# Kernel optimization log

Hardware: AMD Instinct MI355X
Metric: run time of the kernel (lower is better)

## Reference

```python
import jax, jax.numpy as jnp
import numpy as np

NEG_SLOPE = 0.2  # PyG GATConv default negative_slope


def gat_conv(x, edge_index, W, att_src, att_dst, bias):
    # PyG GATConv, heads=1, add_self_loops=True, lin bias=False, final bias added
    N = x.shape[0]
    h = x @ W                                     # [N, F]
    loops = jnp.arange(N, dtype=edge_index.dtype)
    src = jnp.concatenate([edge_index[0], loops])
    dst = jnp.concatenate([edge_index[1], loops])
    a_src = h @ att_src                           # [N]
    a_dst = h @ att_dst                           # [N]
    e = a_src[src] + a_dst[dst]
    e = jnp.where(e > 0, e, NEG_SLOPE * e)        # leaky_relu
    m = jax.ops.segment_max(e, dst, num_segments=N)
    w = jnp.exp(e - m[dst])
    denom = jax.ops.segment_sum(w, dst, num_segments=N)
    alpha = w / denom[dst]
    out = jax.ops.segment_sum(h[src] * alpha[:, None], dst, num_segments=N)
    return out + bias


def gcn_conv(x, edge_index, W, b):
    # PyG GCNConv: add self-loops + symmetric normalization
    N = x.shape[0]
    loops = jnp.arange(N, dtype=edge_index.dtype)
    src = jnp.concatenate([edge_index[0], loops])
    dst = jnp.concatenate([edge_index[1], loops])
    deg = jax.ops.segment_sum(jnp.ones(src.shape[0], dtype=x.dtype), dst, num_segments=N)
    dinv = jax.lax.rsqrt(jnp.maximum(deg, 1e-12))  # deg >= 1 thanks to self-loops
    norm = dinv[src] * dinv[dst]
    xw = x @ W
    return jax.ops.segment_sum(xw[src] * norm[:, None], dst, num_segments=N) + b


def get_final_node(x, batch, num_graphs):
    nn_ = jax.ops.segment_sum(jnp.ones(x.shape[0], dtype=jnp.int32), batch, num_segments=num_graphs)
    cum = jnp.concatenate([jnp.zeros(1, dtype=nn_.dtype), jnp.cumsum(nn_)[:-1]])
    return x[cum]


def ontology_emb(table, e1, e2, W, asrc, adst, b, idx_map):
    emb = gat_conv(table, e1, W, asrc, adst, b)
    emb = gat_conv(emb, e2, W, asrc, adst, b)
    return emb[idx_map]


def _forward(spec_emb, diag_table, proce_table, atc_table,
             diag_W, diag_asrc, diag_adst, diag_b,
             proce_W, proce_asrc, proce_adst, proce_b,
             atc_W, atc_asrc, atc_adst, atc_b,
             gcn_W1, gcn_b1, gcn_W2, gcn_b2, gcn_W3, gcn_b3,
             diag_e1, diag_e2, proce_e1, proce_e2, atc_e1, atc_e2,
             diag_map, proce_map, atc_map,
             left_x, left_graph_index, right_x, right_graph_index,
             left_x_batch, right_x_batch, num_graphs):
    diag_emb = ontology_emb(diag_table, diag_e1, diag_e2, diag_W, diag_asrc, diag_adst, diag_b, diag_map)
    proce_emb = ontology_emb(proce_table, proce_e1, proce_e2, proce_W, proce_asrc, proce_adst, proce_b, proce_map)
    atc_emb = ontology_emb(atc_table, atc_e1, atc_e2, atc_W, atc_asrc, atc_adst, atc_b, atc_map)
    all_emb = jnp.concatenate([spec_emb, diag_emb, proce_emb, atc_emb], axis=0)
    lh = all_emb[left_x[:, 0]]   # squeeze(dim=1)
    rh = all_emb[right_x[:, 0]]
    for W, b in ((gcn_W1, gcn_b1), (gcn_W2, gcn_b2), (gcn_W3, gcn_b3)):
        lh = gcn_conv(lh, left_graph_index, W, b)
        rh = gcn_conv(rh, right_graph_index, W, b)
    lf = get_final_node(lh, left_x_batch, num_graphs)
    rf = get_final_node(rh, right_x_batch, num_graphs)
    eps = 1e-6  # CosineSimilarity eps
    num = jnp.sum(lf * rf, axis=-1)
    den = jnp.maximum(jnp.linalg.norm(lf, axis=-1), eps) * jnp.maximum(jnp.linalg.norm(rf, axis=-1), eps)
    return num / den


def setup_inputs() -> dict:
    key = jax.random.key(0)
    ks = jax.random.split(key, 32)
    HID = 128
    B, NPG = 2048, 50
    N = B * NPG               # 102400 nodes per side
    E_PAT = 409600            # 4 edges per node
    DIAG_N, DIAG_L = 30000, 20000
    PROCE_N, PROCE_L = 12000, 8000
    ATC_N, ATC_L = 6000, 4000
    ALL = 1 + DIAG_L + PROCE_L + ATC_L
    f = lambda k, s: jax.random.normal(k, s, dtype=jnp.float32)
    scale = 0.1
    inp = {
        'spec_emb': f(ks[0], (1, HID)),
        'diag_table': f(ks[1], (DIAG_N, HID)),
        'proce_table': f(ks[2], (PROCE_N, HID)),
        'atc_table': f(ks[3], (ATC_N, HID)),
    }
    for i, nm in enumerate(['diag', 'proce', 'atc']):
        inp[nm + '_W'] = f(ks[4 + i], (HID, HID)) * scale
        inp[nm + '_asrc'] = f(ks[7 + i], (HID,)) * scale
        inp[nm + '_adst'] = f(ks[10 + i], (HID,)) * scale
        inp[nm + '_b'] = jnp.zeros((HID,), jnp.float32)
    for j in range(3):
        inp['gcn_W%d' % (j + 1)] = f(ks[13 + j], (HID, HID)) * scale
        inp['gcn_b%d' % (j + 1)] = jnp.zeros((HID,), jnp.float32)
    inp['diag_e1'] = jax.random.randint(ks[16], (2, DIAG_N), 0, DIAG_N, dtype=jnp.int32)
    inp['diag_e2'] = jax.random.randint(ks[17], (2, DIAG_N), 0, DIAG_N, dtype=jnp.int32)
    inp['proce_e1'] = jax.random.randint(ks[18], (2, PROCE_N), 0, PROCE_N, dtype=jnp.int32)
    inp['proce_e2'] = jax.random.randint(ks[19], (2, PROCE_N), 0, PROCE_N, dtype=jnp.int32)
    inp['atc_e1'] = jax.random.randint(ks[20], (2, ATC_N), 0, ATC_N, dtype=jnp.int32)
    inp['atc_e2'] = jax.random.randint(ks[21], (2, ATC_N), 0, ATC_N, dtype=jnp.int32)
    inp['diag_map'] = jnp.arange(DIAG_L, dtype=jnp.int32)
    inp['proce_map'] = jnp.arange(PROCE_L, dtype=jnp.int32)
    inp['atc_map'] = jnp.arange(ATC_L, dtype=jnp.int32)
    inp['left_x'] = jax.random.randint(ks[22], (N, 1), 0, ALL, dtype=jnp.int32)
    inp['right_x'] = jax.random.randint(ks[23], (N, 1), 0, ALL, dtype=jnp.int32)
    inp['left_graph_index'] = jax.random.randint(ks[24], (2, E_PAT), 0, N, dtype=jnp.int32)
    inp['right_graph_index'] = jax.random.randint(ks[25], (2, E_PAT), 0, N, dtype=jnp.int32)
    batch = jnp.repeat(jnp.arange(B, dtype=jnp.int32), NPG)
    inp['left_x_batch'] = batch
    inp['right_x_batch'] = batch
    inp['num_graphs'] = B
    return inp


def reference(spec_emb, diag_table, proce_table, atc_table,
              diag_W, diag_asrc, diag_adst, diag_b,
              proce_W, proce_asrc, proce_adst, proce_b,
              atc_W, atc_asrc, atc_adst, atc_b,
              gcn_W1, gcn_b1, gcn_W2, gcn_b2, gcn_W3, gcn_b3,
              diag_e1, diag_e2, proce_e1, proce_e2, atc_e1, atc_e2,
              diag_map, proce_map, atc_map,
              left_x, left_graph_index, right_x, right_graph_index,
              left_x_batch, right_x_batch, num_graphs):
    return _forward(spec_emb, diag_table, proce_table, atc_table,
                    diag_W, diag_asrc, diag_adst, diag_b,
                    proce_W, proce_asrc, proce_adst, proce_b,
                    atc_W, atc_asrc, atc_adst, atc_b,
                    gcn_W1, gcn_b1, gcn_W2, gcn_b2, gcn_W3, gcn_b3,
                    diag_e1, diag_e2, proce_e1, proce_e2, atc_e1, atc_e2,
                    diag_map, proce_map, atc_map,
                    left_x, left_graph_index, right_x, right_graph_index,
                    left_x_batch, right_x_batch, num_graphs)
```

## Files before the change

kernel.cpp:

```cpp
#include <hip/hip_runtime.h>
#include <hip/hip_bf16.h>

#define HID 128

typedef unsigned int uint;
typedef unsigned short ushort;
typedef short short8 __attribute__((ext_vector_type(8)));
typedef float f32x4 __attribute__((ext_vector_type(4)));

static inline int cdiv_i(long a, long b) { return (int)((a + b - 1) / b); }
static inline int imax_i(int a, int b) { return a > b ? a : b; }

__device__ __forceinline__ float bf2f(uint hi) {
    return __builtin_bit_cast(float, hi << 16);
}
__device__ __forceinline__ ushort f2bf(float f) {
    uint u = __builtin_bit_cast(uint, f);
    u = (u + 0x7fffu + ((u >> 16) & 1u)) >> 16;
    return (ushort)u;
}

struct CsrDesc {
    const int* esrc[8];
    const int* edst[8];
    int ebase[9];
    int nbase[9];
    int totE;
};

__device__ __forceinline__ void stage_wt(const ushort* __restrict__ Wt,
                                         ushort* __restrict__ wl) {
    const int t = threadIdx.x;
    const int row = t >> 1, half = (t & 1) * 64;
    const uint4* src = (const uint4*)(Wt + row * 128 + half);
    uint4* dst = (uint4*)(wl + row * 136 + half);
#pragma unroll
    for (int i = 0; i < 8; ++i) dst[i] = src[i];
}

template <typename AT>
__device__ __forceinline__ void load_afrag(const AT* __restrict__ A, long row,
                                           int koff, short8& af) {
    if constexpr (__is_same(AT, ushort)) {
        const uint4 raw = *(const uint4*)(A + row * 128 + koff);
        af = __builtin_bit_cast(short8, raw);
    } else {
        const float4* p = (const float4*)(A + row * 128 + koff);
        const float4 x0 = p[0], x1 = p[1];
        af[0] = (short)f2bf(x0.x); af[1] = (short)f2bf(x0.y);
        af[2] = (short)f2bf(x0.z); af[3] = (short)f2bf(x0.w);
        af[4] = (short)f2bf(x1.x); af[5] = (short)f2bf(x1.y);
        af[6] = (short)f2bf(x1.z); af[7] = (short)f2bf(x1.w);
    }
}

struct GOnto {
    const ushort* Wt0; const ushort* Wt1; const ushort* Wt2;
    const float* s0; const float* s1; const float* s2;
    const float* d0; const float* d1; const float* d2;
    int bs1, bs2;
    int r1, r2, r3;
};

template <typename AT>
__device__ void gemm_onto_dev(int b, const AT* __restrict__ x0,
                              const AT* __restrict__ x1, const AT* __restrict__ x2,
                              const GOnto& g, ushort* __restrict__ H,
                              float* __restrict__ as_o, float* __restrict__ ad_o,
                              ushort* __restrict__ wl) {
    const int gid = (b >= g.bs1) + (b >= g.bs2);
    const ushort* Wt = (gid == 0) ? g.Wt0 : (gid == 1) ? g.Wt1 : g.Wt2;
    const float* avs = (gid == 0) ? g.s0 : (gid == 1) ? g.s1 : g.s2;
    const float* avd = (gid == 0) ? g.d0 : (gid == 1) ? g.d1 : g.d2;
    const AT* Ag = (gid == 0) ? x0 : (gid == 1) ? x1 : x2;
    const int bloc = b - ((gid == 0) ? 0 : (gid == 1) ? g.bs1 : g.bs2);
    const long rb = (gid == 0) ? 0 : (gid == 1) ? g.r1 : g.r2;
    const long Mg = ((gid == 0) ? g.r1 : (gid == 1) ? g.r2 : g.r3) - rb;
    stage_wt(Wt, wl);
    __syncthreads();

    const int tid = threadIdx.x;
    const int wave = tid >> 6, lane = tid & 63;
    const int r = lane & 15, q = lane >> 4;
    const long m0 = (long)bloc * 128 + wave * 32;

    f32x4 acc[2][8];
#pragma unroll
    for (int mi = 0; mi < 2; ++mi)
#pragma unroll
        for (int ni = 0; ni < 8; ++ni) acc[mi][ni] = (f32x4)0.f;

#pragma unroll
    for (int t = 0; t < 4; ++t) {
        const int koff = t * 32 + q * 8;
        short8 bfr[8];
#pragma unroll
        for (int ni = 0; ni < 8; ++ni) {
            const uint4 raw = *(const uint4*)(&wl[(ni * 16 + r) * 136 + koff]);
            bfr[ni] = __builtin_bit_cast(short8, raw);
        }
#pragma unroll
        for (int mi = 0; mi < 2; ++mi) {
            long row = m0 + mi * 16 + r;
            if (row >= Mg) row = Mg - 1;
            short8 af;
            load_afrag<AT>(Ag, row, koff, af);
#pragma unroll
            for (int ni = 0; ni < 8; ++ni)
                acc[mi][ni] = __builtin_amdgcn_mfma_f32_16x16x32_bf16(
                    af, bfr[ni], acc[mi][ni], 0, 0, 0);
        }
    }

    ushort* Hg = H + rb * 128;
#pragma unroll
    for (int mi = 0; mi < 2; ++mi) {
#pragma unroll
        for (int ni = 0; ni < 8; ++ni) {
            const int col = ni * 16 + r;
#pragma unroll
            for (int reg = 0; reg < 4; ++reg) {
                const long row = m0 + mi * 16 + q * 4 + reg;
                if (row < Mg) Hg[row * 128 + col] = f2bf(acc[mi][ni][reg]);
            }
        }
    }

    float asv[8], adv[8];
#pragma unroll
    for (int ni = 0; ni < 8; ++ni) {
        asv[ni] = avs[ni * 16 + r];
        adv[ni] = avd[ni * 16 + r];
    }
#pragma unroll
    for (int mi = 0; mi < 2; ++mi) {
#pragma unroll
        for (int reg = 0; reg < 4; ++reg) {
            float ps = 0.f, pd = 0.f;
#pragma unroll
            for (int ni = 0; ni < 8; ++ni) {
                ps += acc[mi][ni][reg] * asv[ni];
                pd += acc[mi][ni][reg] * adv[ni];
            }
#pragma unroll
            for (int o = 1; o < 16; o <<= 1) {
                ps += __shfl_xor(ps, o);
                pd += __shfl_xor(pd, o);
            }
            const long row = m0 + mi * 16 + q * 4 + reg;
            if (r == 0 && row < Mg) {
                as_o[rb + row] = ps;
                ad_o[rb + row] = pd;
            }
        }
    }
}

__global__ __launch_bounds__(256) void gemm_onto_l2(const ushort* __restrict__ x0,
                                                    const ushort* __restrict__ x1,
                                                    const ushort* __restrict__ x2,
                                                    GOnto g, ushort* __restrict__ H,
                                                    float* __restrict__ as_o,
                                                    float* __restrict__ ad_o) {
    __shared__ ushort wl[128 * 136];
    gemm_onto_dev<ushort>(blockIdx.x, x0, x1, x2, g, H, as_o, ad_o, wl);
}

struct EmbSrc {
    const float* spec; const ushort* oE;
    const int* m0; const int* m1; const int* m2;
    int lb2, lb3, r1, r2;
};

__device__ __forceinline__ short8 load_emb(const EmbSrc& e, long row, int koff) {
    short8 af;
    if (row == 0) {
        const float4* pp = (const float4*)(e.spec + koff);
        const float4 x0 = pp[0], x1 = pp[1];
        af[0] = (short)f2bf(x0.x); af[1] = (short)f2bf(x0.y);
        af[2] = (short)f2bf(x0.z); af[3] = (short)f2bf(x0.w);
        af[4] = (short)f2bf(x1.x); af[5] = (short)f2bf(x1.y);
        af[6] = (short)f2bf(x1.z); af[7] = (short)f2bf(x1.w);
        return af;
    }
    const int r = (int)row;
    const int seg = (r >= e.lb2) + (r >= e.lb3);
    const int local = r - ((seg == 0) ? 1 : (seg == 1) ? e.lb2 : e.lb3);
    const int* mp = (seg == 0) ? e.m0 : (seg == 1) ? e.m1 : e.m2;
    const int rb = (seg == 0) ? 0 : (seg == 1) ? e.r1 : e.r2;
    const long sr = (long)rb + mp[local];
    return __builtin_bit_cast(short8, *(const uint4*)(e.oE + sr * 128 + koff));
}

__device__ void gemm_pat_tile(const EmbSrc& es, const ushort* __restrict__ wl,
                              ushort* __restrict__ C, long m0blk, long rowEnd) {
    const int tid = threadIdx.x;
    const int wave = tid >> 6, lane = tid & 63;
    const int r = lane & 15, q = lane >> 4;
    const long m0 = m0blk + wave * 32;

    f32x4 acc[2][8];
#pragma unroll
    for (int mi = 0; mi < 2; ++mi)
#pragma unroll
        for (int ni = 0; ni < 8; ++ni) acc[mi][ni] = (f32x4)0.f;

#pragma unroll
    for (int t = 0; t < 4; ++t) {
        const int koff = t * 32 + q * 8;
        short8 bfr[8];
#pragma unroll
        for (int ni = 0; ni < 8; ++ni) {
            const uint4 raw = *(const uint4*)(&wl[(ni * 16 + r) * 136 + koff]);
            bfr[ni] = __builtin_bit_cast(short8, raw);
        }
#pragma unroll
        for (int mi = 0; mi < 2; ++mi) {
            long row = m0 + mi * 16 + r;
            if (row >= rowEnd) row = rowEnd - 1;
            const short8 af = load_emb(es, row, koff);
#pragma unroll
            for (int ni = 0; ni < 8; ++ni)
                acc[mi][ni] = __builtin_amdgcn_mfma_f32_16x16x32_bf16(
                    af, bfr[ni], acc[mi][ni], 0, 0, 0);
        }
    }

#pragma unroll
    for (int mi = 0; mi < 2; ++mi) {
#pragma unroll
        for (int ni = 0; ni < 8; ++ni) {
            const int col = ni * 16 + r;
#pragma unroll
            for (int reg = 0; reg < 4; ++reg) {
                const long row = m0 + mi * 16 + q * 4 + reg;
                if (row < rowEnd) C[row * 128 + col] = f2bf(acc[mi][ni][reg]);
            }
        }
    }
}

__global__ __launch_bounds__(256) void gemm_pat(EmbSrc es,
                                                const ushort* __restrict__ Wt,
                                                ushort* __restrict__ C, int M) {
    __shared__ ushort wl[128 * 136];
    stage_wt(Wt, wl);
    __syncthreads();
    const long m0 = (long)blockIdx.x * 256;
    gemm_pat_tile(es, wl, C, m0, M);
    if (m0 + 128 < M) gemm_pat_tile(es, wl, C, m0 + 128, M);
}

__device__ __forceinline__ void fold1_dev(int idx, const float* __restrict__ W2,
                                          const float* __restrict__ b2,
                                          const float* __restrict__ W3,
                                          float* __restrict__ W23b) {
    if (idx >= 129 * 128) return;
    const int i = idx >> 7, j = idx & 127;
    const float* a = (i < 128) ? (W2 + i * 128) : b2;
    float s = 0.f;
#pragma unroll 8
    for (int k = 0; k < 128; ++k) s += a[k] * W3[k * 128 + j];
    W23b[idx] = s;
}

__device__ __forceinline__ void fold2_dev(int idx, const float* __restrict__ W1,
                                          const float* __restrict__ b1,
                                          const float* __restrict__ W23b,
                                          ushort* __restrict__ WpT,
                                          float* __restrict__ cbuf) {
    if (idx >= 130 * 128) return;
    const int i = idx >> 7, j = idx & 127;
    if (i == 129) { cbuf[128 + j] = W23b[128 * 128 + j]; return; }
    const float* a = (i < 128) ? (W1 + i * 128) : b1;
    float s = 0.f;
#pragma unroll 8
    for (int k = 0; k < 128; ++k) s += a[k] * W23b[k * 128 + j];
    if (i < 128) WpT[j * 128 + i] = f2bf(s);
    else cbuf[j] = s;
}

__device__ __forceinline__ void mark_dev(int i, const int* __restrict__ lEg,
                                         const int* __restrict__ rEg, int EP,
                                         int NP, int* __restrict__ mk,
                                         int testBit, int setBit) {
    int src, dst;
    if (i < 2 * EP) {
        const int side = i >= EP;
        const int e = i - side * EP;
        const int* eg = side ? rEg : lEg;
        src = side * NP + eg[e];
        dst = side * NP + eg[EP + e];
    } else if (i < 2 * EP + 2 * NP) {
        src = dst = i - 2 * EP;
    } else return;
    if (mk[dst] & testBit) atomicOr(&mk[src], setBit);
}

__device__ __forceinline__ void csr_count_dev(int i, const CsrDesc& d,
                                              int* __restrict__ cnt,
                                              int* __restrict__ pos) {
    if (i >= d.totE) return;
    int li = 0;
#pragma unroll
    for (int k = 1; k < 8; ++k) li += (i >= d.ebase[k]);
    const int v = d.nbase[li] + d.edst[li][i - d.ebase[li]];
    pos[i] = atomicAdd(&cnt[v], 1);
}

struct PackPrep {
    const float* W2; const float* b2; const float* W3; float* W23b;
    const float* wsrc[3]; ushort* wt_out;
    int* cnt; int NV;
    const int* bL; const int* bR; int NP;
    int* gfL; int* gfR; int* mk;
    int nbF1, nbWT, nbInit;
};

__global__ __launch_bounds__(256) void k_prep(PackPrep p) {
    const int b = blockIdx.x, tid = threadIdx.x;
    if (b < p.nbF1) {
        fold1_dev(b * 256 + tid, p.W2, p.b2, p.W3, p.W23b);
    } else if (b < p.nbF1 + p.nbWT) {
        const int idx = (b - p.nbF1) * 256 + tid;
        if (idx < 3 * 16384) {
            const int m = idx >> 14;
            const int e = idx & 16383;
            const int n = e >> 7, k = e & 127;
            p.wt_out[idx] = f2bf(p.wsrc[m][k * 128 + n]);
        }
    } else {
        const int i = (b - p.nbF1 - p.nbWT) * 256 + tid;
        if (i < p.NV) p.cnt[i] = 0;
        if (i < 2 * p.NP) {
            const int side = i >= p.NP;
            const int ii = i - (side ? p.NP : 0);
            const int* bb = side ? p.bR : p.bL;
            int* gf = side ? p.gfR : p.gfL;
            const int cur = bb[ii];
            const int prev = (ii == 0) ? -1 : bb[ii - 1];
            int m = 0;
            if (cur > prev) {
                for (int g = prev + 1; g <= cur; ++g) gf[g] = ii;
                m = 1;
            }
            p.mk[i] = m;
        }
    }
}

struct PackA {
    const float* W1; const float* b1; const float* W23b;
    ushort* WpT; float* cbuf;
    CsrDesc dsc; int* cnt; int* pos;
    const int* lEg; const int* rEg; int EP; int NP; int* mk;
    const float* x0; const float* x1; const float* x2;
    GOnto go; ushort* H; float* as_o; float* ad_o;
    int nbF2, nbCnt, nbMark;
};

__global__ __launch_bounds__(256) void k_packA(PackA p) {
    __shared__ ushort wl[128 * 136];
    const int b = blockIdx.x, tid = threadIdx.x;
    if (b < p.nbF2) {
        fold2_dev(b * 256 + tid, p.W1, p.b1, p.W23b, p.WpT, p.cbuf);
    } else if (b < p.nbF2 + p.nbCnt) {
        csr_count_dev((b - p.nbF2) * 256 + tid, p.dsc, p.cnt, p.pos);
    } else if (b < p.nbF2 + p.nbCnt + p.nbMark) {
        mark_dev((b - p.nbF2 - p.nbCnt) * 256 + tid, p.lEg, p.rEg, p.EP, p.NP,
                 p.mk, 1, 2);
    } else {
        gemm_onto_dev<float>(b - p.nbF2 - p.nbCnt - p.nbMark, p.x0, p.x1, p.x2,
                             p.go, p.H, p.as_o, p.ad_o, wl);
    }
}

struct PackB {
    const int* cnt; int* offs; int* bsum;
    int NV; int pn0; int pcnt; float* dinv;
    const int* lEg; const int* rEg; int EP; int NP; int* mk;
    int nbScan;
};

__device__ void scan_tile_dev(const int* __restrict__ in, int* __restrict__ out,
                              int* __restrict__ bsum, int n, int pn0, int pcnt,
                              float* __restrict__ dinv, int tb, int tid,
                              int* sbuf) {
    const int base = tb * 1024 + tid * 4;
    int v[4];
    int s = 0;
#pragma unroll
    for (int k = 0; k < 4; ++k) {
        const int i = base + k;
        v[k] = (i < n) ? (in[i] + 1) : 0;
        if (i >= pn0 && i < pn0 + pcnt)
            dinv[i - pn0] = rsqrtf(fmaxf((float)v[k], 1e-12f));
        s += v[k];
    }
    sbuf[tid] = s;
    __syncthreads();
    int x = s;
    for (int o = 1; o < 256; o <<= 1) {
        const int t = (tid >= o) ? sbuf[tid - o] : 0;
        __syncthreads();
        x += t;
        sbuf[tid] = x;
        __syncthreads();
    }
    int run = x - s;
#pragma unroll
    for (int k = 0; k < 4; ++k) {
        const int i = base + k;
        if (i < n) out[i] = run;
        run += v[k];
    }
    if (tid == 255) bsum[tb] = x;
}

__global__ __launch_bounds__(256) void k_packB(PackB p) {
    __shared__ int sbuf[256];
    const int b = blockIdx.x, tid = threadIdx.x;
    if (b < p.nbScan) {
        scan_tile_dev(p.cnt, p.offs, p.bsum, p.NV, p.pn0, p.pcnt, p.dinv, b,
                      tid, sbuf);
    } else {
        mark_dev((b - p.nbScan) * 256 + tid, p.lEg, p.rEg, p.EP, p.NP, p.mk, 2, 4);
    }
}

__global__ __launch_bounds__(256) void k_scanfin(int* __restrict__ out,
                                                 const int* __restrict__ bsum,
                                                 int n, int nbData) {
    __shared__ int sbuf[256];
    const int tb = blockIdx.x, tid = threadIdx.x;
    int pLim = tb < nbData ? tb : nbData;
    int pth = 0;
    for (int j = tid; j < pLim; j += 256) pth += bsum[j];
    sbuf[tid] = pth;
    __syncthreads();
    for (int o = 128; o > 0; o >>= 1) {
        if (tid < o) sbuf[tid] += sbuf[tid + o];
        __syncthreads();
    }
    const int prefix = sbuf[0];
    const int base = tb * 1024 + tid * 4;
#pragma unroll
    for (int k = 0; k < 4; ++k) {
        const int i = base + k;
        if (i < n) out[i] += prefix;
        else if (i == n) out[i] = prefix + ((tb < nbData) ? bsum[tb] : 0);
    }
}

__global__ void csr_fill_b(CsrDesc d, const int* __restrict__ offs,
                           const int* __restrict__ pos, const int* __restrict__ cnt,
                           int* __restrict__ srcl, int4* __restrict__ pedge,
                           const float* __restrict__ dinv,
                           const int* __restrict__ lx, const int* __restrict__ rx,
                           const int* __restrict__ mk,
                           int NP, int NV, int pB) {
    const int i = blockIdx.x * 256 + threadIdx.x;
    int v, s, li, idx;
    if (i < d.totE) {
        li = 0;
#pragma unroll
        for (int k = 1; k < 8; ++k) li += (i >= d.ebase[k]);
        const int j = i - d.ebase[li];
        v = d.nbase[li] + d.edst[li][j];
        s = d.esrc[li][j];
        idx = offs[v] + pos[i];
    } else if (i < d.totE + NV) {
        v = i - d.totE;
        li = 0;
#pragma unroll
        for (int k = 1; k < 8; ++k) li += (v >= d.nbase[k]);
        s = v - d.nbase[li];
        idx = offs[v] + cnt[v];
    } else return;
    if (li >= 6) {
        const int n2l = v - d.nbase[6];
        if (mk[n2l] == 0) return;
        const int sg = (li - 6) * NP + s;
        int4 rec;
        rec.x = sg;
        rec.y = (li == 7 ? rx : lx)[s];
        rec.z = __float_as_int(dinv[n2l] * dinv[sg]);
        rec.w = 0;
        pedge[idx - pB] = rec;
    } else {
        srcl[idx] = s;
    }
}

struct GatP {
    int r1, r2;
    int ob0, ob1, ob2;
    const float* b0; const float* b1; const float* b2;
};

__device__ __forceinline__ void acc8(float* acc, float w, const uint4 v) {
    acc[0] += w * bf2f(v.x & 0xffff);
    acc[1] += w * bf2f(v.x >> 16);
    acc[2] += w * bf2f(v.y & 0xffff);
    acc[3] += w * bf2f(v.y >> 16);
    acc[4] += w * bf2f(v.z & 0xffff);
    acc[5] += w * bf2f(v.z >> 16);
    acc[6] += w * bf2f(v.w & 0xffff);
    acc[7] += w * bf2f(v.w >> 16);
}

__global__ __launch_bounds__(256) void gat_all(const ushort* __restrict__ h,
                                               const float* __restrict__ as,
                                               const float* __restrict__ ad,
                                               const int* __restrict__ offs,
                                               const int* __restrict__ srcl,
                                               GatP p, ushort* __restrict__ out,
                                               int Mtot) {
    const int node = blockIdx.x * 16 + (threadIdx.x >> 4);
    const int ql = threadIdx.x & 15;
    if (node >= Mtot) return;
    const int gid = (node >= p.r1) + (node >= p.r2);
    const int rb = (gid == 0) ? 0 : (gid == 1) ? p.r1 : p.r2;
    const int ob = (gid == 0) ? p.ob0 : (gid == 1) ? p.ob1 : p.ob2;
    const float* bias = (gid == 0) ? p.b0 : (gid == 1) ? p.b1 : p.b2;
    const int local = node - rb;
    const int beg = offs[ob + local], end = offs[ob + local + 1];
    const float adv = ad[node];
    float m = -1e30f;
    for (int j = beg; j < end; ++j) {
        float e = as[rb + srcl[j]] + adv;
        e = (e > 0.f) ? e : 0.2f * e;
        m = fmaxf(m, e);
    }
    float denom = 0.f;
    float acc[8] = {0.f, 0.f, 0.f, 0.f, 0.f, 0.f, 0.f, 0.f};
    int j = beg;
    for (; j + 2 <= end; j += 2) {
        const int s0 = srcl[j], s1 = srcl[j + 1];
        float e0 = as[rb + s0] + adv; e0 = (e0 > 0.f) ? e0 : 0.2f * e0;
        float e1 = as[rb + s1] + adv; e1 = (e1 > 0.f) ? e1 : 0.2f * e1;
        const float w0 = __expf(e0 - m), w1 = __expf(e1 - m);
        const uint4 v0 = *(const uint4*)(h + (size_t)(rb + s0) * 128 + ql * 8);
        const uint4 v1 = *(const uint4*)(h + (size_t)(rb + s1) * 128 + ql * 8);
        denom += w0 + w1;
        acc8(acc, w0, v0);
        acc8(acc, w1, v1);
    }
    if (j < end) {
        const int s0 = srcl[j];
        float e0 = as[rb + s0] + adv; e0 = (e0 > 0.f) ? e0 : 0.2f * e0;
        const float w0 = __expf(e0 - m);
        const uint4 v0 = *(const uint4*)(h + (size_t)(rb + s0) * 128 + ql * 8);
        denom += w0;
        acc8(acc, w0, v0);
    }
    const float inv = 1.f / denom;
    const float4 bv0 = *(const float4*)(bias + ql * 8);
    const float4 bv1 = *(const float4*)(bias + ql * 8 + 4);
    uint4 o;
    o.x = (uint)f2bf(acc[0] * inv + bv0.x) | ((uint)f2bf(acc[1] * inv + bv0.y) << 16);
    o.y = (uint)f2bf(acc[2] * inv + bv0.z) | ((uint)f2bf(acc[3] * inv + bv0.w) << 16);
    o.z = (uint)f2bf(acc[4] * inv + bv1.x) | ((uint)f2bf(acc[5] * inv + bv1.y) << 16);
    o.w = (uint)f2bf(acc[6] * inv + bv1.z) | ((uint)f2bf(acc[7] * inv + bv1.w) << 16);
    *(uint4*)(out + (size_t)node * 128 + ql * 8) = o;
}

__global__ __launch_bounds__(256) void gcn_agg1(const ushort* __restrict__ A3,
                                                const int4* __restrict__ pedge,
                                                const int* __restrict__ offs6,
                                                const float* __restrict__ c1,
                                                ushort* __restrict__ t1,
                                                const int* __restrict__ mk,
                                                int NP2, int pB) {
    const int n2 = blockIdx.x * 16 + (threadIdx.x >> 4);
    const int ql = threadIdx.x & 15;
    if (n2 >= NP2) return;
    if ((mk[n2] & 4) == 0) return;
    const int beg = offs6[n2] - pB, end = offs6[n2 + 1] - pB;
    float acc[8] = {0.f, 0.f, 0.f, 0.f, 0.f, 0.f, 0.f, 0.f};
    int j = beg;
    for (; j + 2 <= end; j += 2) {
        const int4 r0 = pedge[j], r1 = pedge[j + 1];
        const float w0 = __int_as_float(r0.z), w1 = __int_as_float(r1.z);
        const uint4 v0 = *(const uint4*)(A3 + (size_t)r0.y * 128 + ql * 8);
        const uint4 v1 = *(const uint4*)(A3 + (size_t)r1.y * 128 + ql * 8);
        acc8(acc, w0, v0);
        acc8(acc, w1, v1);
    }
    if (j < end) {
        const int4 r0 = pedge[j];
        const uint4 v0 = *(const uint4*)(A3 + (size_t)r0.y * 128 + ql * 8);
        acc8(acc, __int_as_float(r0.z), v0);
    }
    const float4 bv0 = *(const float4*)(c1 + ql * 8);
    const float4 bv1 = *(const float4*)(c1 + ql * 8 + 4);
    uint4 o;
    o.x = (uint)f2bf(acc[0] + bv0.x) | ((uint)f2bf(acc[1] + bv0.y) << 16);
    o.y = (uint)f2bf(acc[2] + bv0.z) | ((uint)f2bf(acc[3] + bv0.w) << 16);
    o.z = (uint)f2bf(acc[4] + bv1.x) | ((uint)f2bf(acc[5] + bv1.y) << 16);
    o.w = (uint)f2bf(acc[6] + bv1.z) | ((uint)f2bf(acc[7] + bv1.w) << 16);
    *(uint4*)(t1 + (size_t)n2 * 128 + ql * 8) = o;
}

__device__ __forceinline__ void gcn_q_acc(const ushort* __restrict__ x,
                                          const int4* __restrict__ pedge,
                                          int beg, int end, int ql, float* acc) {
    int j = beg;
    for (; j + 2 <= end; j += 2) {
        const int4 r0 = pedge[j], r1 = pedge[j + 1];
        const float w0 = __int_as_float(r0.z), w1 = __int_as_float(r1.z);
        const uint4 v0 = *(const uint4*)(x + (size_t)r0.x * 128 + ql * 8);
        const uint4 v1 = *(const uint4*)(x + (size_t)r1.x * 128 + ql * 8);
        acc8(acc, w0, v0);
        acc8(acc, w1, v1);
    }
    if (j < end) {
        const int4 r0 = pedge[j];
        const uint4 v0 = *(const uint4*)(x + (size_t)r0.x * 128 + ql * 8);
        acc8(acc, __int_as_float(r0.z), v0);
    }
}

__global__ __launch_bounds__(256) void gcn_agg2(const ushort* __restrict__ t1,
                                                const int4* __restrict__ pedge,
                                                const int* __restrict__ offs6,
                                                const float* __restrict__ c2,
                                                ushort* __restrict__ t2,
                                                const int* __restrict__ mk,
                                                int NP2, int pB) {
    const int n2 = blockIdx.x * 16 + (threadIdx.x >> 4);
    const int ql = threadIdx.x & 15;
    if (n2 >= NP2) return;
    if ((mk[n2] & 2) == 0) return;
    const int beg = offs6[n2] - pB, end = offs6[n2 + 1] - pB;
    float acc[8] = {0.f, 0.f, 0.f, 0.f, 0.f, 0.f, 0.f, 0.f};
    gcn_q_acc(t1, pedge, beg, end, ql, acc);
    const float4 bv0 = *(const float4*)(c2 + ql * 8);
    const float4 bv1 = *(const float4*)(c2 + ql * 8 + 4);
    uint4 o;
    o.x = (uint)f2bf(acc[0] + bv0.x) | ((uint)f2bf(acc[1] + bv0.y) << 16);
    o.y = (uint)f2bf(acc[2] + bv0.z) | ((uint)f2bf(acc[3] + bv0.w) << 16);
    o.z = (uint)f2bf(acc[4] + bv1.x) | ((uint)f2bf(acc[5] + bv1.y) << 16);
    o.w = (uint)f2bf(acc[6] + bv1.z) | ((uint)f2bf(acc[7] + bv1.w) << 16);
    *(uint4*)(t2 + (size_t)n2 * 128 + ql * 8) = o;
}

__global__ __launch_bounds__(256) void final_cos(const ushort* __restrict__ t2,
                                                 const int4* __restrict__ pedge,
                                                 const int* __restrict__ offs6,
                                                 const int* __restrict__ gfL,
                                                 const int* __restrict__ gfR,
                                                 const float* __restrict__ b3,
                                                 float* __restrict__ out,
                                                 int B, int NP, int pB) {
    const int g = blockIdx.x * 8 + (threadIdx.x >> 5);
    const int l32 = threadIdx.x & 31;
    const int side = l32 >> 4;
    const int ql = l32 & 15;
    if (g >= B) return;
    const int n2 = (side ? NP : 0) + (side ? gfR : gfL)[g];
    const int beg = offs6[n2] - pB, end = offs6[n2 + 1] - pB;
    float acc[8] = {0.f, 0.f, 0.f, 0.f, 0.f, 0.f, 0.f, 0.f};
    gcn_q_acc(t2, pedge, beg, end, ql, acc);
    const float4 bv0 = *(const float4*)(b3 + ql * 8);
    const float4 bv1 = *(const float4*)(b3 + ql * 8 + 4);
    float v[8];
    v[0] = acc[0] + bv0.x; v[1] = acc[1] + bv0.y;
    v[2] = acc[2] + bv0.z; v[3] = acc[3] + bv0.w;
    v[4] = acc[4] + bv1.x; v[5] = acc[5] + bv1.y;
    v[6] = acc[6] + bv1.z; v[7] = acc[7] + bv1.w;
    float num = 0.f, nself = 0.f, nother = 0.f;
#pragma unroll
    for (int j = 0; j < 8; ++j) {
        const float o = __shfl_xor(v[j], 16);
        num += v[j] * o;
        nself += v[j] * v[j];
        nother += o * o;
    }
#pragma unroll
    for (int o1 = 1; o1 < 16; o1 <<= 1) {
        num += __shfl_xor(num, o1);
        nself += __shfl_xor(nself, o1);
        nother += __shfl_xor(nother, o1);
    }
    if (l32 == 0)
        out[g] = num / (fmaxf(sqrtf(nself), 1e-6f) * fmaxf(sqrtf(nother), 1e-6f));
}

extern "C" void kernel_launch(void* const* d_in, const int* in_sizes, int n_in,
                              void* d_out, int out_size, void* d_ws, size_t ws_size,
                              hipStream_t stream) {
    (void)n_in; (void)ws_size;
    const float* spec = (const float*)d_in[0];
    const float* tabs[3] = {(const float*)d_in[1], (const float*)d_in[2], (const float*)d_in[3]};
    const float* ontW[3] = {(const float*)d_in[4], (const float*)d_in[8], (const float*)d_in[12]};
    const float* ontAs[3] = {(const float*)d_in[5], (const float*)d_in[9], (const float*)d_in[13]};
    const float* ontAd[3] = {(const float*)d_in[6], (const float*)d_in[10], (const float*)d_in[14]};
    const float* ontB[3] = {(const float*)d_in[7], (const float*)d_in[11], (const float*)d_in[15]};
    const float* gcnW[3] = {(const float*)d_in[16], (const float*)d_in[18], (const float*)d_in[20]};
    const float* gcnB[3] = {(const float*)d_in[17], (const float*)d_in[19], (const float*)d_in[21]};
    const int* e1s[3] = {(const int*)d_in[22], (const int*)d_in[24], (const int*)d_in[26]};
    const int* e2s[3] = {(const int*)d_in[23], (const int*)d_in[25], (const int*)d_in[27]};
    const int* maps[3] = {(const int*)d_in[28], (const int*)d_in[29], (const int*)d_in[30]};
    const int* left_x = (const int*)d_in[31];
    const int* right_x = (const int*)d_in[32];
    const int* left_eg = (const int*)d_in[33];
    const int* right_eg = (const int*)d_in[34];
    const int* left_batch = (const int*)d_in[35];
    const int* right_batch = (const int*)d_in[36];

    int Ms[3] = {in_sizes[1] / HID, in_sizes[2] / HID, in_sizes[3] / HID};
    int E1s[3] = {in_sizes[22] / 2, in_sizes[24] / 2, in_sizes[26] / 2};
    int E2s[3] = {in_sizes[23] / 2, in_sizes[25] / 2, in_sizes[27] / 2};
    int Ls[3] = {in_sizes[28], in_sizes[29], in_sizes[30]};
    const int NP = in_sizes[31];
    const int EP = in_sizes[33] / 2;
    const int B = out_size;
    const long ALL = 1 + (long)Ls[0] + Ls[1] + Ls[2];
    const int Mtot = Ms[0] + Ms[1] + Ms[2];
    const int r1 = Ms[0], r2 = Ms[0] + Ms[1];

    CsrDesc dsc;
    int eCnt[8], nCnt[8];
    for (int i = 0; i < 3; ++i) {
        dsc.esrc[2 * i] = e1s[i];     dsc.edst[2 * i] = e1s[i] + E1s[i];
        dsc.esrc[2 * i + 1] = e2s[i]; dsc.edst[2 * i + 1] = e2s[i] + E2s[i];
        eCnt[2 * i] = E1s[i]; eCnt[2 * i + 1] = E2s[i];
        nCnt[2 * i] = Ms[i];  nCnt[2 * i + 1] = Ms[i];
    }
    dsc.esrc[6] = left_eg;  dsc.edst[6] = left_eg + EP;  eCnt[6] = EP; nCnt[6] = NP;
    dsc.esrc[7] = right_eg; dsc.edst[7] = right_eg + EP; eCnt[7] = EP; nCnt[7] = NP;
    dsc.ebase[0] = 0;
    int nb_acc = 0;
    for (int i = 0; i < 8; ++i) {
        dsc.ebase[i + 1] = dsc.ebase[i] + eCnt[i];
        dsc.nbase[i] = nb_acc;
        nb_acc += nCnt[i];
    }
    const int NV = nb_acc;
    dsc.nbase[8] = NV;
    dsc.totE = dsc.ebase[8];
    const int totEntries = dsc.totE + NV;
    const int pB = dsc.ebase[6] + dsc.nbase[6];
    const int pEntries = totEntries - pB;

    char* ws = (char*)d_ws;
    size_t off = 0;
    auto alloc = [&](size_t bytes) -> void* {
        off = (off + 255) & ~(size_t)255;
        void* p = ws + off;
        off += bytes;
        return p;
    };
    ushort* wt4 = (ushort*)alloc((size_t)4 * 16384 * 2);
    float* W23b = (float*)alloc((size_t)129 * 128 * 4);
    float* cbuf = (float*)alloc((size_t)256 * 4);
    ushort* A3 = (ushort*)alloc((size_t)ALL * HID * 2);
    int* cnt = (int*)alloc((size_t)NV * 4);
    int* offs = (int*)alloc((size_t)(NV + 1) * 4);
    int* pos = (int*)alloc((size_t)dsc.totE * 4);
    int* srcl = (int*)alloc((size_t)pB * 4);
    int4* pedge = (int4*)alloc((size_t)pEntries * 16);
    int* bsum = (int*)alloc(1025 * 4);
    float* dinv = (float*)alloc((size_t)2 * NP * 4);
    float* as = (float*)alloc((size_t)Mtot * 4);
    float* ad = (float*)alloc((size_t)Mtot * 4);
    int* gfL = (int*)alloc((size_t)(B + 1) * 4);
    int* gfR = (int*)alloc((size_t)(B + 1) * 4);
    int* mk = (int*)alloc((size_t)2 * NP * 4);
    ushort* t1 = (ushort*)alloc((size_t)2 * NP * HID * 2);
    ushort* big = (ushort*)alloc((size_t)2 * NP * HID * 2);
    ushort* hbuf = big;
    ushort* obuf = big + (size_t)Mtot * HID;
    ushort* t2 = big;

    const ushort* wtOnt[3] = {wt4, wt4 + 16384, wt4 + 2 * 16384};
    ushort* WpT = wt4 + 3 * 16384;
    const float* c1 = cbuf;
    const float* c2 = cbuf + 128;

    PackPrep pp;
    pp.W2 = gcnW[1]; pp.b2 = gcnB[1]; pp.W3 = gcnW[2]; pp.W23b = W23b;
    pp.wsrc[0] = ontW[0]; pp.wsrc[1] = ontW[1]; pp.wsrc[2] = ontW[2];
    pp.wt_out = wt4;
    pp.cnt = cnt; pp.NV = NV;
    pp.bL = left_batch; pp.bR = right_batch; pp.NP = NP;
    pp.gfL = gfL; pp.gfR = gfR; pp.mk = mk;
    pp.nbF1 = cdiv_i(129 * 128, 256);
    pp.nbWT = cdiv_i(3 * 16384, 256);
    pp.nbInit = cdiv_i(imax_i(NV, 2 * NP), 256);
    k_prep<<<pp.nbF1 + pp.nbWT + pp.nbInit, 256, 0, stream>>>(pp);

    GOnto go;
    go.Wt0 = wtOnt[0]; go.Wt1 = wtOnt[1]; go.Wt2 = wtOnt[2];
    go.s0 = ontAs[0]; go.s1 = ontAs[1]; go.s2 = ontAs[2];
    go.d0 = ontAd[0]; go.d1 = ontAd[1]; go.d2 = ontAd[2];
    go.bs1 = cdiv_i(Ms[0], 128);
    go.bs2 = go.bs1 + cdiv_i(Ms[1], 128);
    const int totBlk = go.bs2 + cdiv_i(Ms[2], 128);
    go.r1 = r1; go.r2 = r2; go.r3 = Mtot;

    PackA pa;
    pa.W1 = gcnW[0]; pa.b1 = gcnB[0]; pa.W23b = W23b;
    pa.WpT = WpT; pa.cbuf = cbuf;
    pa.dsc = dsc; pa.cnt = cnt; pa.pos = pos;
    pa.lEg = left_eg; pa.rEg = right_eg; pa.EP = EP; pa.NP = NP; pa.mk = mk;
    pa.x0 = tabs[0]; pa.x1 = tabs[1]; pa.x2 = tabs[2];
    pa.go = go; pa.H = hbuf; pa.as_o = as; pa.ad_o = ad;
    pa.nbF2 = cdiv_i(130 * 128, 256);
    pa.nbCnt = cdiv_i(dsc.totE, 256);
    pa.nbMark = cdiv_i(2 * EP + 2 * NP, 256);
    k_packA<<<pa.nbF2 + pa.nbCnt + pa.nbMark + totBlk, 256, 0, stream>>>(pa);

    PackB pb;
    pb.cnt = cnt; pb.offs = offs; pb.bsum = bsum;
    pb.NV = NV; pb.pn0 = dsc.nbase[6]; pb.pcnt = 2 * NP; pb.dinv = dinv;
    pb.lEg = left_eg; pb.rEg = right_eg; pb.EP = EP; pb.NP = NP; pb.mk = mk;
    pb.nbScan = cdiv_i(NV, 1024);
    k_packB<<<pb.nbScan + pa.nbMark, 256, 0, stream>>>(pb);

    k_scanfin<<<cdiv_i(NV + 1, 1024), 256, 0, stream>>>(offs, bsum, NV, pb.nbScan);

    csr_fill_b<<<cdiv_i(totEntries, 256), 256, 0, stream>>>(dsc, offs, pos, cnt,
                                                            srcl, pedge, dinv,
                                                            left_x, right_x, mk,
                                                            NP, NV, pB);

    const GatP gp0{r1, r2, dsc.nbase[0], dsc.nbase[2], dsc.nbase[4],
                   ontB[0], ontB[1], ontB[2]};
    gat_all<<<cdiv_i(Mtot, 16), 256, 0, stream>>>(hbuf, as, ad, offs, srcl, gp0,
                                                  obuf, Mtot);
    gemm_onto_l2<<<totBlk, 256, 0, stream>>>(obuf, obuf + (size_t)r1 * HID,
                                             obuf + (size_t)r2 * HID, go, hbuf,
                                             as, ad);
    const GatP gp1{r1, r2, dsc.nbase[1], dsc.nbase[3], dsc.nbase[5],
                   ontB[0], ontB[1], ontB[2]};
    gat_all<<<cdiv_i(Mtot, 16), 256, 0, stream>>>(hbuf, as, ad, offs, srcl, gp1,
                                                  obuf, Mtot);

    EmbSrc es;
    es.spec = spec; es.oE = obuf;
    es.m0 = maps[0]; es.m1 = maps[1]; es.m2 = maps[2];
    es.lb2 = 1 + Ls[0]; es.lb3 = 1 + Ls[0] + Ls[1];
    es.r1 = r1; es.r2 = r2;
    gemm_pat<<<cdiv_i(ALL, 256), 256, 0, stream>>>(es, WpT, A3, (int)ALL);

    const int* offs6 = offs + dsc.nbase[6];
    gcn_agg1<<<cdiv_i(2 * NP, 16), 256, 0, stream>>>(A3, pedge, offs6, c1, t1,
                                                     mk, 2 * NP, pB);
    gcn_agg2<<<cdiv_i(2 * NP, 16), 256, 0, stream>>>(t1, pedge, offs6, c2, t2,
                                                     mk, 2 * NP, pB);
    final_cos<<<cdiv_i(B, 8), 256, 0, stream>>>(t2, pedge, offs6, gfL, gfR,
                                                gcnB[2], (float*)d_out, B, NP, pB);
}
```

Measured before the change: 361.4 us.

## Regroup launches: move ontology GEMM into scan kernel, fuse patient CSR fill with GAT

The first-layer ontology GEMM moves out of the initial scatter/count kernel and into the kernel that runs the prefix scan and second marking pass. The CSR fill is split in two: ontology-graph edges are filled first, and patient-graph edges are filled inside the same launch as the first GAT layer. The goal is to balance work across launches and to overlap independent fill work with GAT aggregation. This costs an extra launch for the split fill and larger block-heterogeneous kernels.

```diff
diff --git a/kernel.cpp b/kernel.cpp
--- a/kernel.cpp
+++ b/kernel.cpp
@@ -349,38 +349,25 @@
     }
 }
 
-struct PackA {
+struct PackScatter {
     const float* W1; const float* b1; const float* W23b;
     ushort* WpT; float* cbuf;
     CsrDesc dsc; int* cnt; int* pos;
     const int* lEg; const int* rEg; int EP; int NP; int* mk;
-    const float* x0; const float* x1; const float* x2;
-    GOnto go; ushort* H; float* as_o; float* ad_o;
     int nbF2, nbCnt, nbMark;
 };
 
-__global__ __launch_bounds__(256) void k_packA(PackA p) {
-    __shared__ ushort wl[128 * 136];
+__global__ __launch_bounds__(256) void k_scatter(PackScatter p) {
     const int b = blockIdx.x, tid = threadIdx.x;
     if (b < p.nbF2) {
         fold2_dev(b * 256 + tid, p.W1, p.b1, p.W23b, p.WpT, p.cbuf);
     } else if (b < p.nbF2 + p.nbCnt) {
         csr_count_dev((b - p.nbF2) * 256 + tid, p.dsc, p.cnt, p.pos);
-    } else if (b < p.nbF2 + p.nbCnt + p.nbMark) {
+    } else {
         mark_dev((b - p.nbF2 - p.nbCnt) * 256 + tid, p.lEg, p.rEg, p.EP, p.NP,
                  p.mk, 1, 2);
-    } else {
-        gemm_onto_dev<float>(b - p.nbF2 - p.nbCnt - p.nbMark, p.x0, p.x1, p.x2,
-                             p.go, p.H, p.as_o, p.ad_o, wl);
-    }
-}
-
-struct PackB {
-    const int* cnt; int* offs; int* bsum;
-    int NV; int pn0; int pcnt; float* dinv;
-    const int* lEg; const int* rEg; int EP; int NP; int* mk;
-    int nbScan;
-};
+    }
+}
 
 __device__ void scan_tile_dev(const int* __restrict__ in, int* __restrict__ out,
                               int* __restrict__ bsum, int n, int pn0, int pcnt,
@@ -417,14 +404,27 @@
     if (tid == 255) bsum[tb] = x;
 }
 
-__global__ __launch_bounds__(256) void k_packB(PackB p) {
-    __shared__ int sbuf[256];
+struct PackMid {
+    const float* x0; const float* x1; const float* x2;
+    GOnto go; ushort* H; float* as_o; float* ad_o;
+    const int* cnt; int* offs; int* bsum;
+    int NV; int pn0; int pcnt; float* dinv;
+    const int* lEg; const int* rEg; int EP; int NP; int* mk;
+    int nbGemm, nbScan;
+};
+
+__global__ __launch_bounds__(256) void k_mid(PackMid p) {
+    __shared__ uint smem4[128 * 136 / 2];
     const int b = blockIdx.x, tid = threadIdx.x;
-    if (b < p.nbScan) {
-        scan_tile_dev(p.cnt, p.offs, p.bsum, p.NV, p.pn0, p.pcnt, p.dinv, b,
-                      tid, sbuf);
+    if (b < p.nbGemm) {
+        gemm_onto_dev<float>(b, p.x0, p.x1, p.x2, p.go, p.H, p.as_o, p.ad_o,
+                             (ushort*)smem4);
+    } else if (b < p.nbGemm + p.nbScan) {
+        scan_tile_dev(p.cnt, p.offs, p.bsum, p.NV, p.pn0, p.pcnt, p.dinv,
+                      b - p.nbGemm, tid, (int*)smem4);
     } else {
-        mark_dev((b - p.nbScan) * 256 + tid, p.lEg, p.rEg, p.EP, p.NP, p.mk, 2, 4);
+        mark_dev((b - p.nbGemm - p.nbScan) * 256 + tid, p.lEg, p.rEg, p.EP,
+                 p.NP, p.mk, 2, 4);
     }
 }
 
@@ -452,44 +452,51 @@
     }
 }
 
-__global__ void csr_fill_b(CsrDesc d, const int* __restrict__ offs,
-                           const int* __restrict__ pos, const int* __restrict__ cnt,
-                           int* __restrict__ srcl, int4* __restrict__ pedge,
-                           const float* __restrict__ dinv,
-                           const int* __restrict__ lx, const int* __restrict__ rx,
-                           const int* __restrict__ mk,
-                           int NP, int NV, int pB) {
-    const int i = blockIdx.x * 256 + threadIdx.x;
-    int v, s, li, idx;
-    if (i < d.totE) {
+struct FillP {
+    CsrDesc dsc;
+    const int* offs; const int* pos; const int* cnt;
+    int* srcl; int4* pedge; const float* dinv;
+    const int* lx; const int* rx; const int* mk;
+    int NP, pB;
+    int eStart, eCount, vStart, vCount;
+};
+
+__device__ void fill_dev(const FillP& f, int idx) {
+    int v, s, li, cidx;
+    if (idx < f.eCount) {
+        const int i = f.eStart + idx;
         li = 0;
 #pragma unroll
-        for (int k = 1; k < 8; ++k) li += (i >= d.ebase[k]);
-        const int j = i - d.ebase[li];
-        v = d.nbase[li] + d.edst[li][j];
-        s = d.esrc[li][j];
-        idx = offs[v] + pos[i];
-    } else if (i < d.totE + NV) {
-        v = i - d.totE;
+        for (int k = 1; k < 8; ++k) li += (i >= f.dsc.ebase[k]);
+        const int j = i - f.dsc.ebase[li];
+        v = f.dsc.nbase[li] + f.dsc.edst[li][j];
+        s = f.dsc.esrc[li][j];
+        cidx = f.offs[v] + f.pos[i];
+    } else if (idx < f.eCount + f.vCount) {
+        v = f.vStart + (idx - f.eCount);
         li = 0;
 #pragma unroll
-        for (int k = 1; k < 8; ++k) li += (v >= d.nbase[k]);
-        s = v - d.nbase[li];
-        idx = offs[v] + cnt[v];
+        for (int k = 1; k < 8; ++k) li += (v >= f.dsc.nbase[k]);
+        s = v - f.dsc.nbase[li];
+        cidx = f.offs[v] + f.cnt[v];
     } else return;
     if (li >= 6) {
-        const int n2l = v - d.nbase[6];
-        if (mk[n2l] == 0) return;
-        const int sg = (li - 6) * NP + s;
+        const int n2l = v - f.dsc.nbase[6];
+        if (f.mk[n2l] == 0) return;
+        const int sg = (li - 6) * f.NP + s;
         int4 rec;
         rec.x = sg;
-        rec.y = (li == 7 ? rx : lx)[s];
-        rec.z = __float_as_int(dinv[n2l] * dinv[sg]);
+        rec.y = (li == 7 ? f.rx : f.lx)[s];
+        rec.z = __float_as_int(f.dinv[n2l] * f.dinv[sg]);
         rec.w = 0;
-        pedge[idx - pB] = rec;
+        f.pedge[cidx - f.pB] = rec;
     } else {
-        srcl[idx] = s;
-    }
+        f.srcl[cidx] = s;
+    }
+}
+
+__global__ __launch_bounds__(256) void k_fill(FillP f) {
+    fill_dev(f, blockIdx.x * 256 + threadIdx.x);
 }
 
 struct GatP {
@@ -509,15 +516,10 @@
     acc[7] += w * bf2f(v.w >> 16);
 }
 
-__global__ __launch_bounds__(256) void gat_all(const ushort* __restrict__ h,
-                                               const float* __restrict__ as,
-                                               const float* __restrict__ ad,
-                                               const int* __restrict__ offs,
-                                               const int* __restrict__ srcl,
-                                               GatP p, ushort* __restrict__ out,
-                                               int Mtot) {
-    const int node = blockIdx.x * 16 + (threadIdx.x >> 4);
-    const int ql = threadIdx.x & 15;
+__device__ void gat_dev(int node, int ql, const ushort* __restrict__ h,
+                        const float* __restrict__ as, const float* __restrict__ ad,
+                        const int* __restrict__ offs, const int* __restrict__ srcl,
+                        const GatP& p, ushort* __restrict__ out, int Mtot) {
     if (node >= Mtot) return;
     const int gid = (node >= p.r1) + (node >= p.r2);
     const int rb = (gid == 0) ? 0 : (gid == 1) ? p.r1 : p.r2;
@@ -563,6 +565,34 @@
     o.z = (uint)f2bf(acc[4] * inv + bv1.x) | ((uint)f2bf(acc[5] * inv + bv1.y) << 16);
     o.w = (uint)f2bf(acc[6] * inv + bv1.z) | ((uint)f2bf(acc[7] * inv + bv1.w) << 16);
     *(uint4*)(out + (size_t)node * 128 + ql * 8) = o;
+}
+
+__global__ __launch_bounds__(256) void gat_all(const ushort* __restrict__ h,
+                                               const float* __restrict__ as,
+                                               const float* __restrict__ ad,
+                                               const int* __restrict__ offs,
+                                               const int* __restrict__ srcl,
+                                               GatP p, ushort* __restrict__ out,
+                                               int Mtot) {
+    gat_dev(blockIdx.x * 16 + (threadIdx.x >> 4), threadIdx.x & 15, h, as, ad,
+            offs, srcl, p, out, Mtot);
+}
+
+struct GatFill {
+    const ushort* h; const float* as; const float* ad;
+    const int* offs; const int* srcl;
+    GatP gp; ushort* out; int Mtot; int nbGat;
+    FillP f;
+};
+
+__global__ __launch_bounds__(256) void k_gat_fill(GatFill g) {
+    const int b = blockIdx.x, tid = threadIdx.x;
+    if (b < g.nbGat) {
+        gat_dev(b * 16 + (tid >> 4), tid & 15, g.h, g.as, g.ad, g.offs, g.srcl,
+                g.gp, g.out, g.Mtot);
+    } else {
+        fill_dev(g.f, (b - g.nbGat) * 256 + tid);
+    }
 }
 
 __global__ __launch_bounds__(256) void gcn_agg1(const ushort* __restrict__ A3,
@@ -800,36 +830,51 @@
     const int totBlk = go.bs2 + cdiv_i(Ms[2], 128);
     go.r1 = r1; go.r2 = r2; go.r3 = Mtot;
 
-    PackA pa;
-    pa.W1 = gcnW[0]; pa.b1 = gcnB[0]; pa.W23b = W23b;
-    pa.WpT = WpT; pa.cbuf = cbuf;
-    pa.dsc = dsc; pa.cnt = cnt; pa.pos = pos;
-    pa.lEg = left_eg; pa.rEg = right_eg; pa.EP = EP; pa.NP = NP; pa.mk = mk;
-    pa.x0 = tabs[0]; pa.x1 = tabs[1]; pa.x2 = tabs[2];
-    pa.go = go; pa.H = hbuf; pa.as_o = as; pa.ad_o = ad;
-    pa.nbF2 = cdiv_i(130 * 128, 256);
-    pa.nbCnt = cdiv_i(dsc.totE, 256);
-    pa.nbMark = cdiv_i(2 * EP + 2 * NP, 256);
-    k_packA<<<pa.nbF2 + pa.nbCnt + pa.nbMark + totBlk, 256, 0, stream>>>(pa);
-
-    PackB pb;
-    pb.cnt = cnt; pb.offs = offs; pb.bsum = bsum;
-    pb.NV = NV; pb.pn0 = dsc.nbase[6]; pb.pcnt = 2 * NP; pb.dinv = dinv;
-    pb.lEg = left_eg; pb.rEg = right_eg; pb.EP = EP; pb.NP = NP; pb.mk = mk;
-    pb.nbScan = cdiv_i(NV, 1024);
-    k_packB<<<pb.nbScan + pa.nbMark, 256, 0, stream>>>(pb);
-
-    k_scanfin<<<cdiv_i(NV + 1, 1024), 256, 0, stream>>>(offs, bsum, NV, pb.nbScan);
-
-    csr_fill_b<<<cdiv_i(totEntries, 256), 256, 0, stream>>>(dsc, offs, pos, cnt,
-                                                            srcl, pedge, dinv,
-                                                            left_x, right_x, mk,
-                                                            NP, NV, pB);
-
-    const GatP gp0{r1, r2, dsc.nbase[0], dsc.nbase[2], dsc.nbase[4],
-                   ontB[0], ontB[1], ontB[2]};
-    gat_all<<<cdiv_i(Mtot, 16), 256, 0, stream>>>(hbuf, as, ad, offs, srcl, gp0,
-                                                  obuf, Mtot);
+    PackScatter psc;
+    psc.W1 = gcnW[0]; psc.b1 = gcnB[0]; psc.W23b = W23b;
+    psc.WpT = WpT; psc.cbuf = cbuf;
+    psc.dsc = dsc; psc.cnt = cnt; psc.pos = pos;
+    psc.lEg = left_eg; psc.rEg = right_eg; psc.EP = EP; psc.NP = NP; psc.mk = mk;
+    psc.nbF2 = cdiv_i(130 * 128, 256);
+    psc.nbCnt = cdiv_i(dsc.totE, 256);
+    psc.nbMark = cdiv_i(2 * EP + 2 * NP, 256);
+    k_scatter<<<psc.nbF2 + psc.nbCnt + psc.nbMark, 256, 0, stream>>>(psc);
+
+    PackMid pm;
+    pm.x0 = tabs[0]; pm.x1 = tabs[1]; pm.x2 = tabs[2];
+    pm.go = go; pm.H = hbuf; pm.as_o = as; pm.ad_o = ad;
+    pm.cnt = cnt; pm.offs = offs; pm.bsum = bsum;
+    pm.NV = NV; pm.pn0 = dsc.nbase[6]; pm.pcnt = 2 * NP; pm.dinv = dinv;
+    pm.lEg = left_eg; pm.rEg = right_eg; pm.EP = EP; pm.NP = NP; pm.mk = mk;
+    pm.nbGemm = totBlk;
+    pm.nbScan = cdiv_i(NV, 1024);
+    k_mid<<<pm.nbGemm + pm.nbScan + psc.nbMark, 256, 0, stream>>>(pm);
+
+    k_scanfin<<<cdiv_i(NV + 1, 1024), 256, 0, stream>>>(offs, bsum, NV, pm.nbScan);
+
+    FillP fb;
+    fb.dsc = dsc; fb.offs = offs; fb.pos = pos; fb.cnt = cnt;
+    fb.srcl = srcl; fb.pedge = pedge; fb.dinv = dinv;
+    fb.lx = left_x; fb.rx = right_x; fb.mk = mk;
+    fb.NP = NP; fb.pB = pB;
+
+    FillP fo = fb;
+    fo.eStart = 0;             fo.eCount = dsc.ebase[6];
+    fo.vStart = 0;             fo.vCount = dsc.nbase[6];
+    k_fill<<<cdiv_i(fo.eCount + fo.vCount, 256), 256, 0, stream>>>(fo);
+
+    GatFill gf;
+    gf.h = hbuf; gf.as = as; gf.ad = ad; gf.offs = offs; gf.srcl = srcl;
+    gf.gp = GatP{r1, r2, dsc.nbase[0], dsc.nbase[2], dsc.nbase[4],
+                 ontB[0], ontB[1], ontB[2]};
+    gf.out = obuf; gf.Mtot = Mtot;
+    gf.nbGat = cdiv_i(Mtot, 16);
+    gf.f = fb;
+    gf.f.eStart = dsc.ebase[6]; gf.f.eCount = dsc.totE - dsc.ebase[6];
+    gf.f.vStart = dsc.nbase[6]; gf.f.vCount = NV - dsc.nbase[6];
+    k_gat_fill<<<gf.nbGat + cdiv_i(gf.f.eCount + gf.f.vCount, 256), 256, 0,
+                 stream>>>(gf);
+
     gemm_onto_l2<<<totBlk, 256, 0, stream>>>(obuf, obuf + (size_t)r1 * HID,
                                              obuf + (size_t)r2 * HID, go, hbuf,
                                              as, ad);
```

Result: no change. 360.9 us (-0.1%).
